# Kernel optimization log

Measured on AMD Instinct MI355X. Metric: run time of the kernel, lower is better.

## Reference

```python
import jax, jax.numpy as jnp
import numpy as np

B = 1024       # number of graphs in batch
N_T = 51200    # junction-tree nodes
N_G = 61440    # molecule atoms
E = 100352     # tree edges = line-graph nodes
E_LG = 200704  # line-graph edges
D = 450        # hidden / feature dim
VOCAB = 780    # junction-tree vocab


def _att(h, a, x, gid, nseg):
    # Attention.forward: per-graph softmax over node scores, weighted sum of x.
    q = (h @ a)[gid]                      # (N, d_x) query broadcast to nodes
    s = jnp.sum(x * q, axis=1)            # (N,)
    m = jax.ops.segment_max(s, gid, num_segments=nseg)
    e = jnp.exp(s - m[gid])
    z = jax.ops.segment_sum(e, gid, num_segments=nseg)
    return jax.ops.segment_sum((e / z[gid])[:, None] * x, gid, num_segments=nseg)


def setup_inputs() -> dict:
    key = jax.random.key(0)
    ks = iter(jax.random.split(key, 48))
    nk = lambda: next(ks)
    p = lambda shape: 0.001 * jax.random.uniform(nk(), shape, dtype=jnp.float32)
    inp = {}
    inp['x_T'] = jax.random.normal(nk(), (N_T, D), jnp.float32)
    inp['x_G'] = jax.random.normal(nk(), (N_G, D), jnp.float32)
    inp['id_onehot'] = jax.random.uniform(nk(), (N_T, VOCAB), dtype=jnp.float32)
    inp['msg0'] = jnp.zeros((E, D), jnp.float32)
    inp['embeddings'] = p((VOCAB, D))
    # TreeGRU params
    for n in ['wz', 'uz', 'wr', 'ur', 'w_h', 'u_h']:
        inp[n] = p((D, D))
    for n in ['bz', 'br', 'b_h']:
        inp[n] = jnp.zeros((1, D), jnp.float32)
    # decoder topology params
    inp['w_d1'] = p((D, D)); inp['w_d2'] = p((D, D)); inp['b_d1'] = jnp.zeros((1, D), jnp.float32)
    inp['a_dT'] = p((D, D)); inp['a_dG'] = p((D, D))
    inp['w_d3'] = p((D, D)); inp['w_d4'] = p((2 * D, D)); inp['b_d2'] = jnp.zeros((1, D), jnp.float32)
    inp['u_d'] = p((D, 1)); inp['b_d3'] = jnp.zeros((1,), jnp.float32)
    # decoder label params
    inp['w_l1'] = p((D, D)); inp['w_l2'] = p((2 * D, D)); inp['b_l1'] = jnp.zeros((1, D), jnp.float32)
    inp['a_lT'] = p((D, D)); inp['a_lG'] = p((D, D))
    inp['u_l'] = p((D, VOCAB)); inp['b_l2'] = jnp.zeros((1, VOCAB), jnp.float32)
    # targets
    inp['topo_target'] = (jax.random.uniform(nk(), (B,)) < 0.5).astype(jnp.float32)
    # graph structure (int)
    inp['edge_src'] = jax.random.randint(nk(), (E,), 0, N_T, jnp.int32)
    inp['edge_dst'] = jax.random.randint(nk(), (E,), 0, N_T, jnp.int32)
    inp['lg_src'] = jax.random.randint(nk(), (E_LG,), 0, E, jnp.int32)
    inp['lg_dst'] = jax.random.randint(nk(), (E_LG,), 0, E, jnp.int32)
    inp['gid_T'] = jnp.sort(jax.random.randint(nk(), (N_T,), 0, B, jnp.int32))
    inp['gid_G'] = jnp.sort(jax.random.randint(nk(), (N_G,), 0, B, jnp.int32))
    inp['root_eids'] = jax.random.randint(nk(), (B,), 0, E, jnp.int32)
    inp['label_target'] = jax.random.randint(nk(), (B,), 0, VOCAB, jnp.int32)
    return inp


def reference(x_T, x_G, id_onehot, msg0, embeddings, wz, uz, bz, wr, ur, br,
              w_h, u_h, b_h, w_d1, w_d2, b_d1, a_dT, a_dG, w_d3, w_d4, b_d2,
              u_d, b_d3, w_l1, w_l2, b_l1, a_lT, a_lG, u_l, b_l2, topo_target,
              edge_src, edge_dst, lg_src, lg_dst, gid_T, gid_G, root_eids,
              label_target):
    seg = jax.ops.segment_sum
    nE = msg0.shape[0]
    f = id_onehot @ embeddings            # Y_T.ndata['f']
    f_src = f[edge_src]                   # per line-graph-node source-node feat
    f_dst = f[edge_dst]
    # ---- TreeGRU over the line graph (full-graph update) ----
    s = seg(msg0[lg_src], lg_dst, num_segments=nE)                 # sum of h_{ki}
    z = jax.nn.sigmoid(f_src @ wz + s @ uz + bz)
    r = jax.nn.sigmoid(f_dst[lg_src] @ wr + msg0[lg_src] @ ur + br)  # per lg-edge
    sum_rh = seg(r * msg0[lg_src], lg_dst, num_segments=nE)
    h_tilde = jnp.tanh(f_src @ w_h + sum_rh @ u_h + b_h)
    msg = (1.0 - z) * s + z * h_tilde                               # new h_{ij}
    # ---- decoder hidden state per edge ----
    sum_h = seg(msg[lg_src], lg_dst, num_segments=nE)
    h = jax.nn.relu(f_src @ w_d1 + sum_h @ w_d2 + b_d1)             # (E, d_h)
    h_root = h[root_eids]                                           # (B, d_h)
    # ---- topology prediction (Eq. 5-6) ----
    c_d = jnp.concatenate([_att(h_root, a_dT, x_T, gid_T, B),
                           _att(h_root, a_dG, x_G, gid_G, B)], axis=1)
    d_logit = (jax.nn.relu(h_root @ w_d3 + c_d @ w_d4 + b_d2) @ u_d + b_d3)[:, 0]
    topology_ce = jnp.sum(jax.nn.softplus(d_logit) - topo_target * d_logit)
    # ---- label prediction (Eq. 8-9) ----
    q = msg[root_eids]                                              # (B, d_msgT)
    c_l = jnp.concatenate([_att(q, a_lT, x_T, gid_T, B),
                           _att(q, a_lG, x_G, gid_G, B)], axis=1)
    l_logits = jax.nn.relu(q @ w_l1 + c_l @ w_l2 + b_l1) @ u_l + b_l2
    lp = jax.nn.log_softmax(l_logits, axis=-1)
    label_ce = -jnp.sum(lp[jnp.arange(B), label_target])
    return jnp.stack([topology_ce, label_ce])
```

## Files before the change

### kernel.cpp

```cpp
#include <hip/hip_runtime.h>
#include <math.h>


#define BGR   1024
#define NT    51200
#define NG    61440
#define NE    100352
#define NELG  200704
#define D     450
#define DP    452
#define CATS  1356
#define VOCAB 780
#define VP    784
#define CAP   4096
#define KC    16
#define SAS   68
#define SWS   68

__device__ __forceinline__ float sigmoidf_(float x) { return 1.0f / (1.0f + expf(-x)); }
__device__ __forceinline__ float softplusf_(float x) {
    return fmaxf(x, 0.0f) + log1pf(expf(-fabsf(x)));
}
__device__ __forceinline__ int lower_bound_i(const int* __restrict__ a, int n, int v) {
    int lo = 0, hi = n;
    while (lo < hi) { int mid = (lo + hi) >> 1; if (a[mid] < v) lo = mid + 1; else hi = mid; }
    return lo;
}
__device__ __forceinline__ float4 g4(const float* p, bool pred) {
    float4 z = make_float4(0.f, 0.f, 0.f, 0.f);
    return pred ? *(const float4*)p : z;
}
__device__ __forceinline__ void loadb4a(const float* __restrict__ b, int c0, int n, float* o) {
#pragma unroll
    for (int i = 0; i < 4; ++i) o[i] = (c0 + i < n) ? b[c0 + i] : 0.f;
}

template <int M>
__device__ __forceinline__ void gemm64(
    const float* __restrict__ A, int ldA, int K, int rowBase, int nRows,
    const int* s_idx, const float* const (&W)[M], int ldW, int Wcols,
    int colBase, float* sA, float* sW, float (&acc)[M][4][4]) {
    const int tid = threadIdx.x;
    const int a_r = tid >> 2, a_k = (tid & 3) << 2;
    const int w_k = tid >> 4, w_c = (tid & 15) << 2;
    const int r0 = (tid & 15) << 2, c0 = (tid >> 4) << 2;
    const bool rok = (rowBase + a_r) < nRows;
    const float* arow;
    {
        int sr = rok ? (s_idx ? s_idx[a_r] : rowBase + a_r) : 0;
        arow = A + (size_t)sr * ldA;
    }
    const int wcol = colBase + w_c;
    const bool cok = (wcol < Wcols);
    const int nch = (K + KC - 1) / KC;
    float4 pa = g4(arow + a_k, rok && (a_k < K));
    float4 pw[M];
#pragma unroll
    for (int m = 0; m < M; ++m)
        pw[m] = g4(W[m] + (size_t)w_k * ldW + wcol, cok && (w_k < K));
    for (int ch = 0; ch < nch; ++ch) {
        __syncthreads();
        sA[(a_k + 0) * SAS + a_r] = pa.x;
        sA[(a_k + 1) * SAS + a_r] = pa.y;
        sA[(a_k + 2) * SAS + a_r] = pa.z;
        sA[(a_k + 3) * SAS + a_r] = pa.w;
#pragma unroll
        for (int m = 0; m < M; ++m)
            *(float4*)&sW[(m * KC + w_k) * SWS + w_c] = pw[m];
        __syncthreads();
        int k0 = (ch + 1) * KC;
        if (ch + 1 < nch) {
            pa = g4(arow + k0 + a_k, rok && (k0 + a_k < K));
#pragma unroll
            for (int m = 0; m < M; ++m)
                pw[m] = g4(W[m] + (size_t)(k0 + w_k) * ldW + wcol, cok && (k0 + w_k < K));
        }
#pragma unroll
        for (int k = 0; k < KC; ++k) {
            float4 av4 = *(const float4*)&sA[k * SAS + r0];
            float ar[4] = { av4.x, av4.y, av4.z, av4.w };
#pragma unroll
            for (int m = 0; m < M; ++m) {
                float4 wv4 = *(const float4*)&sW[(m * KC + k) * SWS + c0];
                float wr[4] = { wv4.x, wv4.y, wv4.z, wv4.w };
#pragma unroll
                for (int i = 0; i < 4; ++i)
#pragma unroll
                    for (int j = 0; j < 4; ++j)
                        acc[m][i][j] = fmaf(ar[i], wr[j], acc[m][i][j]);
            }
        }
    }
}

struct PrepJob { const float* src; float* dst; int srcRows; int srcCols; int ld; int cum; };
struct PrepArgs { PrepJob j[16]; int total; };

__global__ void k_prep(PrepArgs a) {
    int idx = blockIdx.x * blockDim.x + threadIdx.x;
    int stride = gridDim.x * blockDim.x;
    for (; idx < a.total; idx += stride) {
        int jj = 0;
        while (jj < 15 && idx >= a.j[jj + 1].cum) ++jj;
        PrepJob J = a.j[jj];
        int local = idx - J.cum;
        int row = local / J.ld, col = local - row * J.ld;
        float v = (row < J.srcRows && col < J.srcCols) ? J.src[(size_t)row * J.srcCols + col] : 0.f;
        J.dst[local] = v;
    }
}

__global__ void k_init(float* __restrict__ sumh, int* __restrict__ root_slot,
                       int* __restrict__ counter, float* __restrict__ dl,
                       float* __restrict__ out) {
    int i = blockIdx.x * blockDim.x + threadIdx.x;
    if (i < BGR * DP) sumh[i] = 0.0f;
    if (i < NE) root_slot[i] = -1;
    if (i < BGR) dl[i] = 0.0f;
    if (i == 0) counter[0] = 0;
    if (i < 2) out[i] = 0.0f;
}

__global__ void k_scatter_roots(const int* __restrict__ root_eids, int* __restrict__ root_slot) {
    int b = blockIdx.x * blockDim.x + threadIdx.x;
    if (b < BGR) root_slot[root_eids[b]] = b;
}

__global__ void k_build_tasks(const int* __restrict__ lg_src, const int* __restrict__ lg_dst,
                              const int* __restrict__ edge_src, const int* __restrict__ root_slot,
                              int2* __restrict__ tasks, int* __restrict__ counter) {
    int j = blockIdx.x * blockDim.x + threadIdx.x;
    if (j < NELG) {
        int r = root_slot[lg_dst[j]];
        if (r >= 0) {
            int idx = atomicAdd(counter, 1);
            if (idx < CAP) tasks[idx] = make_int2(edge_src[lg_src[j]], r);
        }
    }
}

__global__ __launch_bounds__(256) void kA(
    const float* __restrict__ id_onehot, const float* __restrict__ emb_p,
    const int* __restrict__ edge_src, const int* __restrict__ root_eids,
    const int2* __restrict__ tasks, const int* __restrict__ counter,
    float* __restrict__ f_all) {
    __shared__ float sA[KC * SAS];
    __shared__ float sW[KC * SWS];
    __shared__ int s_idx[64];
    int T = counter[0]; if (T > CAP) T = CAP;
    int nRows = BGR + T;
    int rowBase = blockIdx.x * 64, colBase = blockIdx.y * 64;
    if (rowBase >= nRows) return;
    int tid = threadIdx.x;
    if (tid < 64) {
        int row = rowBase + tid, n = 0;
        if (row < nRows) n = (row < BGR) ? edge_src[root_eids[row]] : tasks[row - BGR].x;
        s_idx[tid] = n;
    }
    __syncthreads();
    float acc[1][4][4] = {};
    const float* W[1] = { emb_p };
    gemm64<1>(id_onehot, VOCAB, VOCAB, rowBase, nRows, s_idx, W, DP, DP, colBase, sA, sW, acc);
    int r0 = (tid & 15) << 2, c0 = (tid >> 4) << 2;
    int cg = colBase + c0;
    if (cg < DP) {
#pragma unroll
        for (int i = 0; i < 4; ++i) {
            int row = rowBase + r0 + i;
            if (row < nRows)
                *(float4*)(f_all + (size_t)row * DP + cg) =
                    make_float4(acc[0][i][0], acc[0][i][1], acc[0][i][2], acc[0][i][3]);
        }
    }
}

__global__ __launch_bounds__(256) void kB(
    const float* __restrict__ f_all,
    const float* __restrict__ wz_p, const float* __restrict__ wh_p, const float* __restrict__ wd1_p,
    const float* __restrict__ bz, const float* __restrict__ b_h,
    const int2* __restrict__ tasks, const int* __restrict__ counter,
    float* __restrict__ catl, float* __restrict__ fw1, float* __restrict__ sumh) {
    __shared__ float sA[KC * SAS];
    __shared__ float sW[3 * KC * SWS];
    int tileR = blockIdx.x, colBase = blockIdx.y * 64;
    int tid = threadIdx.x;
    int r0 = (tid & 15) << 2, c0 = (tid >> 4) << 2;
    int cg = colBase + c0;
    int T = counter[0]; if (T > CAP) T = CAP;
    if (tileR < 16) {
        int rowBase = tileR * 64;
        float acc[3][4][4] = {};
        const float* W[3] = { wz_p, wh_p, wd1_p };
        gemm64<3>(f_all, DP, DP, rowBase, BGR, nullptr, W, DP, DP, colBase, sA, sW, acc);
        if (cg < DP) {
            float bz4[4], bh4[4];
            loadb4a(bz, cg, D, bz4); loadb4a(b_h, cg, D, bh4);
#pragma unroll
            for (int i = 0; i < 4; ++i) {
                int row = rowBase + r0 + i;
                float q[4];
#pragma unroll
                for (int j = 0; j < 4; ++j)
                    q[j] = sigmoidf_(acc[0][i][j] + bz4[j]) * tanhf(acc[1][i][j] + bh4[j]);
                *(float4*)(catl + (size_t)row * CATS + cg) = make_float4(q[0], q[1], q[2], q[3]);
                *(float4*)(fw1 + (size_t)row * DP + cg) =
                    make_float4(acc[2][i][0], acc[2][i][1], acc[2][i][2], acc[2][i][3]);
            }
        }
    } else {
        int rowBase = BGR + (tileR - 16) * 64;
        int nRows = BGR + T;
        if (rowBase >= nRows) return;
        float acc[2][4][4] = {};
        const float* W[2] = { wz_p, wh_p };
        gemm64<2>(f_all, DP, DP, rowBase, nRows, nullptr, W, DP, DP, colBase, sA, sW, acc);
        if (cg < DP) {
            float bz4[4], bh4[4];
            loadb4a(bz, cg, D, bz4); loadb4a(b_h, cg, D, bh4);
#pragma unroll
            for (int i = 0; i < 4; ++i) {
                int row = rowBase + r0 + i;
                if (row < nRows) {
                    int slot = tasks[row - BGR].y;
                    float* dst = sumh + (size_t)slot * DP + cg;
#pragma unroll
                    for (int j = 0; j < 4; ++j)
                        atomicAdd(dst + j, sigmoidf_(acc[0][i][j] + bz4[j]) * tanhf(acc[1][i][j] + bh4[j]));
                }
            }
        }
    }
}

__global__ __launch_bounds__(256) void kC(
    const float* __restrict__ fw1, const float* __restrict__ sumh,
    const int* __restrict__ root_slot, const int* __restrict__ root_eids,
    const float* __restrict__ wd2_p, const float* __restrict__ b_d1,
    float* __restrict__ catd) {
    __shared__ float sA[KC * SAS];
    __shared__ float sW[KC * SWS];
    __shared__ int s_idx[64];
    int rowBase = blockIdx.x * 64, colBase = blockIdx.y * 64;
    int tid = threadIdx.x;
    if (tid < 64) s_idx[tid] = root_slot[root_eids[rowBase + tid]];
    __syncthreads();
    float acc[1][4][4] = {};
    const float* W[1] = { wd2_p };
    gemm64<1>(sumh, DP, DP, rowBase, BGR, s_idx, W, DP, DP, colBase, sA, sW, acc);
    int r0 = (tid & 15) << 2, c0 = (tid >> 4) << 2;
    int cg = colBase + c0;
    if (cg < DP) {
        float bd[4]; loadb4a(b_d1, cg, D, bd);
#pragma unroll
        for (int i = 0; i < 4; ++i) {
            int row = rowBase + r0 + i;
            float4 f1 = *(const float4*)(fw1 + (size_t)row * DP + cg);
            float fr[4] = { f1.x, f1.y, f1.z, f1.w };
            float o[4];
#pragma unroll
            for (int j = 0; j < 4; ++j) o[j] = fmaxf(acc[0][i][j] + fr[j] + bd[j], 0.f);
            *(float4*)(catd + (size_t)row * CATS + cg) = make_float4(o[0], o[1], o[2], o[3]);
        }
    }
}

__global__ __launch_bounds__(256) void kD(
    const float* __restrict__ catd, const float* __restrict__ catl,
    const float* __restrict__ adT_p, const float* __restrict__ adG_p,
    const float* __restrict__ alT_p, const float* __restrict__ alG_p,
    float* __restrict__ qdT, float* __restrict__ qdG,
    float* __restrict__ qlT, float* __restrict__ qlG) {
    __shared__ float sA[KC * SAS];
    __shared__ float sW[2 * KC * SWS];
    int rowBase = blockIdx.x * 64, colBase = blockIdx.y * 64, job = blockIdx.z;
    int tid = threadIdx.x;
    const float* A = job ? catl : catd;
    float acc[2][4][4] = {};
    const float* W[2] = { job ? alT_p : adT_p, job ? alG_p : adG_p };
    gemm64<2>(A, CATS, DP, rowBase, BGR, nullptr, W, DP, DP, colBase, sA, sW, acc);
    int r0 = (tid & 15) << 2, c0 = (tid >> 4) << 2;
    int cg = colBase + c0;
    if (cg < DP) {
        float* oa = job ? qlT : qdT;
        float* ob = job ? qlG : qdG;
#pragma unroll
        for (int i = 0; i < 4; ++i) {
            int row = rowBase + r0 + i;
            *(float4*)(oa + (size_t)row * DP + cg) =
                make_float4(acc[0][i][0], acc[0][i][1], acc[0][i][2], acc[0][i][3]);
            *(float4*)(ob + (size_t)row * DP + cg) =
                make_float4(acc[1][i][0], acc[1][i][1], acc[1][i][2], acc[1][i][3]);
        }
    }
}

__global__ __launch_bounds__(256) void k_att(
    const float* __restrict__ x_T, const float* __restrict__ x_G,
    const int* __restrict__ gid_T, const int* __restrict__ gid_G,
    const float* __restrict__ qdT, const float* __restrict__ qdG,
    const float* __restrict__ qlT, const float* __restrict__ qlG,
    float* __restrict__ catd, float* __restrict__ catl) {
    int bid = blockIdx.x, b = bid & (BGR - 1), which = bid >> 10;
    const float* x   = which ? x_G   : x_T;
    const int*   gid = which ? gid_G : gid_T;
    int N            = which ? NG    : NT;
    const float* qd  = (which ? qdG : qdT) + (size_t)b * DP;
    const float* ql  = (which ? qlG : qlT) + (size_t)b * DP;
    float* ad = catd + (size_t)b * CATS + DP + which * DP;
    float* al = catl + (size_t)b * CATS + DP + which * DP;
    int tid = threadIdx.x, lane = tid & 63, wave = tid >> 6;
    __shared__ float s_qd[D], s_ql[D];
    __shared__ float s_m[4][2], s_z[4][2];
    __shared__ float s_acc[4][2][D];
    for (int d = tid; d < D; d += 256) { s_qd[d] = qd[d]; s_ql[d] = ql[d]; }
    int lo = lower_bound_i(gid, N, b), hi = lower_bound_i(gid, N, b + 1);
    __syncthreads();
    float md = -INFINITY, ml = -INFINITY, zd = 0.0f, zl = 0.0f;
    float accd[8] = {}, accl[8] = {};
    for (int n = lo + wave; n < hi; n += 4) {
        const float* xr = x + (size_t)n * D;
        float vx[8]; float pd = 0.0f, pl = 0.0f;
#pragma unroll
        for (int i = 0; i < 8; ++i) {
            int d = lane + (i << 6);
            float v = (d < D) ? xr[d] : 0.0f;
            vx[i] = v;
            if (d < D) { pd = fmaf(v, s_qd[d], pd); pl = fmaf(v, s_ql[d], pl); }
        }
#pragma unroll
        for (int o = 32; o; o >>= 1) { pd += __shfl_xor(pd, o); pl += __shfl_xor(pl, o); }
        float nmd = fmaxf(md, pd), nml = fmaxf(ml, pl);
        float sd = expf(md - nmd), sl = expf(ml - nml);
        float ed = expf(pd - nmd), el = expf(pl - nml);
        zd = zd * sd + ed; zl = zl * sl + el;
#pragma unroll
        for (int i = 0; i < 8; ++i) {
            accd[i] = fmaf(accd[i], sd, ed * vx[i]);
            accl[i] = fmaf(accl[i], sl, el * vx[i]);
        }
        md = nmd; ml = nml;
    }
#pragma unroll
    for (int i = 0; i < 8; ++i) {
        int d = lane + (i << 6);
        if (d < D) { s_acc[wave][0][d] = accd[i]; s_acc[wave][1][d] = accl[i]; }
    }
    if (lane == 0) { s_m[wave][0] = md; s_m[wave][1] = ml; s_z[wave][0] = zd; s_z[wave][1] = zl; }
    __syncthreads();
    bool nonempty = (hi > lo);
    float Md = fmaxf(fmaxf(s_m[0][0], s_m[1][0]), fmaxf(s_m[2][0], s_m[3][0]));
    float Ml = fmaxf(fmaxf(s_m[0][1], s_m[1][1]), fmaxf(s_m[2][1], s_m[3][1]));
    float scd[4], scl[4];
#pragma unroll
    for (int w = 0; w < 4; ++w) { scd[w] = expf(s_m[w][0] - Md); scl[w] = expf(s_m[w][1] - Ml); }
    float Zd = s_z[0][0] * scd[0] + s_z[1][0] * scd[1] + s_z[2][0] * scd[2] + s_z[3][0] * scd[3];
    float Zl = s_z[0][1] * scl[0] + s_z[1][1] * scl[1] + s_z[2][1] * scl[2] + s_z[3][1] * scl[3];
    for (int d = tid; d < DP; d += 256) {
        bool v = (d < D);
        float adv = 0.f, alv = 0.f;
        if (v && nonempty) {
            adv = (s_acc[0][0][d] * scd[0] + s_acc[1][0][d] * scd[1]
                 + s_acc[2][0][d] * scd[2] + s_acc[3][0][d] * scd[3]) / Zd;
            alv = (s_acc[0][1][d] * scl[0] + s_acc[1][1][d] * scl[1]
                 + s_acc[2][1][d] * scl[2] + s_acc[3][1][d] * scl[3]) / Zl;
        }
        ad[d] = adv; al[d] = alv;
    }
}

__global__ __launch_bounds__(256) void kEF(
    const float* __restrict__ catd, const float* __restrict__ catl,
    const float* __restrict__ wcd_p, const float* __restrict__ wcl_p,
    const float* __restrict__ b_d2, const float* __restrict__ u_d,
    const float* __restrict__ b_l1,
    float* __restrict__ h_l, float* __restrict__ dl) {
    __shared__ float sA[KC * SAS];
    __shared__ float sW[KC * SWS];
    __shared__ float s_dl[64];
    int rowBase = blockIdx.x * 64, colBase = blockIdx.y * 64, job = blockIdx.z;
    int tid = threadIdx.x;
    if (!job && tid < 64) s_dl[tid] = 0.f;
    float acc[1][4][4] = {};
    const float* A = job ? catl : catd;
    const float* W[1] = { job ? wcl_p : wcd_p };
    gemm64<1>(A, CATS, CATS, rowBase, BGR, nullptr, W, DP, DP, colBase, sA, sW, acc);
    int r0 = (tid & 15) << 2, c0 = (tid >> 4) << 2;
    int cg = colBase + c0;
    if (job) {
        if (cg < DP) {
            float b1[4]; loadb4a(b_l1, cg, D, b1);
#pragma unroll
            for (int i = 0; i < 4; ++i) {
                int row = rowBase + r0 + i;
                *(float4*)(h_l + (size_t)row * DP + cg) =
                    make_float4(fmaxf(acc[0][i][0] + b1[0], 0.f), fmaxf(acc[0][i][1] + b1[1], 0.f),
                                fmaxf(acc[0][i][2] + b1[2], 0.f), fmaxf(acc[0][i][3] + b1[3], 0.f));
            }
        }
    } else {
        if (cg < DP) {
            float b2[4], ud[4];
            loadb4a(b_d2, cg, D, b2); loadb4a(u_d, cg, D, ud);
#pragma unroll
            for (int i = 0; i < 4; ++i) {
                float p = 0.f;
#pragma unroll
                for (int j = 0; j < 4; ++j) p += fmaxf(acc[0][i][j] + b2[j], 0.f) * ud[j];
                atomicAdd(&s_dl[r0 + i], p);
            }
        }
        __syncthreads();
        if (tid < 64) atomicAdd(&dl[rowBase + tid], s_dl[tid]);
    }
}

__global__ __launch_bounds__(256) void kG(
    const float* __restrict__ h_l, const float* __restrict__ ul_p,
    const float* __restrict__ b_l2, float* __restrict__ logits) {
    __shared__ float sA[KC * SAS];
    __shared__ float sW[KC * SWS];
    int rowBase = blockIdx.x * 64, colBase = blockIdx.y * 64;
    int tid = threadIdx.x;
    float acc[1][4][4] = {};
    const float* W[1] = { ul_p };
    gemm64<1>(h_l, DP, DP, rowBase, BGR, nullptr, W, VP, VP, colBase, sA, sW, acc);
    int r0 = (tid & 15) << 2, c0 = (tid >> 4) << 2;
    int cg = colBase + c0;
    if (cg < VP) {
        float bl[4]; loadb4a(b_l2, cg, VOCAB, bl);
#pragma unroll
        for (int i = 0; i < 4; ++i) {
            int row = rowBase + r0 + i;
            *(float4*)(logits + (size_t)row * VP + cg) =
                make_float4(acc[0][i][0] + bl[0], acc[0][i][1] + bl[1],
                            acc[0][i][2] + bl[2], acc[0][i][3] + bl[3]);
        }
    }
}

__global__ __launch_bounds__(256) void k_ce(
    const float* __restrict__ logits, const int* __restrict__ label_t,
    float* __restrict__ out) {
    __shared__ float s_red[4];
    int base = blockIdx.x * 4, tid = threadIdx.x, lane = tid & 63, wave = tid >> 6;
    float ce = 0.0f;
    for (int r = 0; r < 4; ++r) {
        const float* lg = logits + (size_t)(base + r) * VP;
        float m = -INFINITY;
        for (int d = tid; d < VOCAB; d += 256) m = fmaxf(m, lg[d]);
#pragma unroll
        for (int o = 32; o; o >>= 1) m = fmaxf(m, __shfl_xor(m, o));
        if (lane == 0) s_red[wave] = m;
        __syncthreads();
        float m4 = fmaxf(fmaxf(s_red[0], s_red[1]), fmaxf(s_red[2], s_red[3]));
        __syncthreads();
        float s = 0.0f;
        for (int d = tid; d < VOCAB; d += 256) s += expf(lg[d] - m4);
#pragma unroll
        for (int o = 32; o; o >>= 1) s += __shfl_xor(s, o);
        if (lane == 0) s_red[wave] = s;
        __syncthreads();
        if (tid == 0) {
            float Z = s_red[0] + s_red[1] + s_red[2] + s_red[3];
            ce += (m4 + logf(Z)) - lg[label_t[base + r]];
        }
        __syncthreads();
    }
    if (tid == 0) atomicAdd(&out[1], ce);
}

__global__ __launch_bounds__(1024) void k_topo_final(
    const float* __restrict__ dl, const float* __restrict__ b_d3,
    const float* __restrict__ topo_t, float* __restrict__ out) {
    __shared__ float s_red[16];
    int tid = threadIdx.x, lane = tid & 63, wave = tid >> 6;
    float v = dl[tid] + b_d3[0];
    float ce = softplusf_(v) - topo_t[tid] * v;
#pragma unroll
    for (int o = 32; o; o >>= 1) ce += __shfl_xor(ce, o);
    if (lane == 0) s_red[wave] = ce;
    __syncthreads();
    if (tid == 0) {
        float s = 0.f;
#pragma unroll
        for (int w = 0; w < 16; ++w) s += s_red[w];
        atomicAdd(&out[0], s);
    }
}

extern "C" void kernel_launch(void* const* d_in, const int* in_sizes, int n_in,
                              void* d_out, int out_size, void* d_ws, size_t ws_size,
                              hipStream_t stream) {
    const float* x_T       = (const float*)d_in[0];
    const float* x_G       = (const float*)d_in[1];
    const float* id_onehot = (const float*)d_in[2];
    const float* emb   = (const float*)d_in[4];
    const float* wz    = (const float*)d_in[5];
    const float* w_h   = (const float*)d_in[9];
    const float* bz    = (const float*)d_in[11];
    const float* b_h   = (const float*)d_in[13];
    const float* w_d1  = (const float*)d_in[14];
    const float* w_d2  = (const float*)d_in[15];
    const float* b_d1  = (const float*)d_in[16];
    const float* a_dT  = (const float*)d_in[17];
    const float* a_dG  = (const float*)d_in[18];
    const float* w_d3  = (const float*)d_in[19];
    const float* w_d4  = (const float*)d_in[20];
    const float* b_d2  = (const float*)d_in[21];
    const float* u_d   = (const float*)d_in[22];
    const float* b_d3  = (const float*)d_in[23];
    const float* w_l1  = (const float*)d_in[24];
    const float* w_l2  = (const float*)d_in[25];
    const float* b_l1  = (const float*)d_in[26];
    const float* a_lT  = (const float*)d_in[27];
    const float* a_lG  = (const float*)d_in[28];
    const float* u_l   = (const float*)d_in[29];
    const float* b_l2  = (const float*)d_in[30];
    const float* topo_t = (const float*)d_in[31];
    const int* edge_src  = (const int*)d_in[32];
    const int* lg_src    = (const int*)d_in[34];
    const int* lg_dst    = (const int*)d_in[35];
    const int* gid_T     = (const int*)d_in[36];
    const int* gid_G     = (const int*)d_in[37];
    const int* root_eids = (const int*)d_in[38];
    const int* label_t   = (const int*)d_in[39];
    float* out = (float*)d_out;

    char* p = (char*)d_ws;
    auto take = [&](size_t bytes) -> char* {
        char* r = p; p += (bytes + 255) & ~(size_t)255; return r;
    };
    const size_t WSQ = (size_t)DP * DP * 4;
    float* wz_p  = (float*)take(WSQ);
    float* wh_p  = (float*)take(WSQ);
    float* wd1_p = (float*)take(WSQ);
    float* wd2_p = (float*)take(WSQ);
    float* adT_p = (float*)take(WSQ);
    float* adG_p = (float*)take(WSQ);
    float* alT_p = (float*)take(WSQ);
    float* alG_p = (float*)take(WSQ);
    float* wcd_p = (float*)take((size_t)CATS * DP * 4);
    float* wcl_p = (float*)take((size_t)CATS * DP * 4);
    float* emb_p = (float*)take((size_t)VOCAB * DP * 4);
    float* ul_p  = (float*)take((size_t)DP * VP * 4);
    float* catd  = (float*)take((size_t)BGR * CATS * 4);
    float* catl  = (float*)take((size_t)BGR * CATS * 4);
    float* f_all = (float*)take((size_t)(BGR + CAP) * DP * 4);
    const size_t BD = (size_t)BGR * DP * 4;
    float* fw1  = (float*)take(BD);
    float* sumh = (float*)take(BD);
    float* h_l  = (float*)take(BD);
    float* qdT  = (float*)take(BD);
    float* qdG  = (float*)take(BD);
    float* qlT  = (float*)take(BD);
    float* qlG  = (float*)take(BD);
    float* logits = qdT;
    float* dl   = (float*)take((size_t)BGR * 4);
    int*  root_slot = (int*)take((size_t)NE * 4);
    int*  counter   = (int*)take(256);
    int2* tasks     = (int2*)take((size_t)CAP * 8);

    PrepArgs pa; int cum = 0;
    auto addjob = [&](int i, const float* src, float* dst, int sr, int sc, int dr, int ld) {
        pa.j[i].src = src; pa.j[i].dst = dst; pa.j[i].srcRows = sr; pa.j[i].srcCols = sc;
        pa.j[i].ld = ld; pa.j[i].cum = cum; cum += dr * ld;
    };
    addjob(0, wz, wz_p, D, D, DP, DP);
    addjob(1, w_h, wh_p, D, D, DP, DP);
    addjob(2, w_d1, wd1_p, D, D, DP, DP);
    addjob(3, w_d2, wd2_p, D, D, DP, DP);
    addjob(4, a_dT, adT_p, D, D, DP, DP);
    addjob(5, a_dG, adG_p, D, D, DP, DP);
    addjob(6, a_lT, alT_p, D, D, DP, DP);
    addjob(7, a_lG, alG_p, D, D, DP, DP);
    addjob(8, w_d3, wcd_p, D, D, DP, DP);
    addjob(9, w_d4, wcd_p + (size_t)DP * DP, D, D, DP, DP);
    addjob(10, w_d4 + (size_t)D * D, wcd_p + (size_t)2 * DP * DP, D, D, DP, DP);
    addjob(11, w_l1, wcl_p, D, D, DP, DP);
    addjob(12, w_l2, wcl_p + (size_t)DP * DP, D, D, DP, DP);
    addjob(13, w_l2 + (size_t)D * D, wcl_p + (size_t)2 * DP * DP, D, D, DP, DP);
    addjob(14, emb, emb_p, VOCAB, D, VOCAB, DP);
    addjob(15, u_l, ul_p, D, VOCAB, DP, VP);
    pa.total = cum;

    k_prep<<<2048, 256, 0, stream>>>(pa);
    k_init<<<(BGR * DP + 255) / 256, 256, 0, stream>>>(sumh, root_slot, counter, dl, out);
    k_scatter_roots<<<(BGR + 255) / 256, 256, 0, stream>>>(root_eids, root_slot);
    k_build_tasks<<<(NELG + 255) / 256, 256, 0, stream>>>(lg_src, lg_dst, edge_src, root_slot, tasks, counter);
    kA<<<dim3((BGR + CAP) / 64, 8), 256, 0, stream>>>(id_onehot, emb_p, edge_src, root_eids,
                                                      tasks, counter, f_all);
    kB<<<dim3(16 + CAP / 64, 8), 256, 0, stream>>>(f_all, wz_p, wh_p, wd1_p, bz, b_h,
                                                   tasks, counter, catl, fw1, sumh);
    kC<<<dim3(16, 8), 256, 0, stream>>>(fw1, sumh, root_slot, root_eids, wd2_p, b_d1, catd);
    kD<<<dim3(16, 8, 2), 256, 0, stream>>>(catd, catl, adT_p, adG_p, alT_p, alG_p,
                                           qdT, qdG, qlT, qlG);
    k_att<<<2 * BGR, 256, 0, stream>>>(x_T, x_G, gid_T, gid_G, qdT, qdG, qlT, qlG, catd, catl);
    kEF<<<dim3(16, 8, 2), 256, 0, stream>>>(catd, catl, wcd_p, wcl_p, b_d2, u_d, b_l1, h_l, dl);
    k_topo_final<<<1, 1024, 0, stream>>>(dl, b_d3, topo_t, out);
    kG<<<dim3(16, VP / 64 + 1, 1), 256, 0, stream>>>(h_l, ul_p, b_l2, logits);
    k_ce<<<BGR / 4, 256, 0, stream>>>(logits, label_t, out);
}
```

Baseline: 941.6 us.

## Replace FP32 SIMT GEMMs with split-bf16 MFMA matrix-core GEMMs

Every dense GEMM stage moves from the shared-memory FP32 FMA tiling to MFMA 16x16x32 bf16 instructions. To keep near-FP32 accuracy, each operand is split into hi and lo bf16 parts and three products are accumulated. Weights are pre-transposed and padded into bf16 hi/lo buffers, and activations are converted the same way between stages. This adds extra conversion kernels and memory traffic, and the MFMA loop reads operands directly from global memory with no LDS staging.

```diff
diff --git a/kernel.cpp b/kernel.cpp
--- a/kernel.cpp
+++ b/kernel.cpp
@@ -9,13 +9,17 @@
 #define NELG  200704
 #define D     450
 #define DP    452
-#define CATS  1356
+#define KP_D  480
+#define KP_V  800
+#define CATP  1440
 #define VOCAB 780
 #define VP    784
 #define CAP   4096
-#define KC    16
-#define SAS   68
-#define SWS   68
+#define WT_N  512
+#define WT_NV 832
+
+typedef short bf16x8 __attribute__((ext_vector_type(8)));
+typedef float f32x4 __attribute__((ext_vector_type(4)));
 
 __device__ __forceinline__ float sigmoidf_(float x) { return 1.0f / (1.0f + expf(-x)); }
 __device__ __forceinline__ float softplusf_(float x) {
@@ -26,87 +30,68 @@
     while (lo < hi) { int mid = (lo + hi) >> 1; if (a[mid] < v) lo = mid + 1; else hi = mid; }
     return lo;
 }
-__device__ __forceinline__ float4 g4(const float* p, bool pred) {
-    float4 z = make_float4(0.f, 0.f, 0.f, 0.f);
-    return pred ? *(const float4*)p : z;
-}
-__device__ __forceinline__ void loadb4a(const float* __restrict__ b, int c0, int n, float* o) {
-#pragma unroll
-    for (int i = 0; i < 4; ++i) o[i] = (c0 + i < n) ? b[c0 + i] : 0.f;
-}
-
-template <int M>
-__device__ __forceinline__ void gemm64(
-    const float* __restrict__ A, int ldA, int K, int rowBase, int nRows,
-    const int* s_idx, const float* const (&W)[M], int ldW, int Wcols,
-    int colBase, float* sA, float* sW, float (&acc)[M][4][4]) {
-    const int tid = threadIdx.x;
-    const int a_r = tid >> 2, a_k = (tid & 3) << 2;
-    const int w_k = tid >> 4, w_c = (tid & 15) << 2;
-    const int r0 = (tid & 15) << 2, c0 = (tid >> 4) << 2;
-    const bool rok = (rowBase + a_r) < nRows;
-    const float* arow;
-    {
-        int sr = rok ? (s_idx ? s_idx[a_r] : rowBase + a_r) : 0;
-        arow = A + (size_t)sr * ldA;
-    }
-    const int wcol = colBase + w_c;
-    const bool cok = (wcol < Wcols);
-    const int nch = (K + KC - 1) / KC;
-    float4 pa = g4(arow + a_k, rok && (a_k < K));
-    float4 pw[M];
-#pragma unroll
-    for (int m = 0; m < M; ++m)
-        pw[m] = g4(W[m] + (size_t)w_k * ldW + wcol, cok && (w_k < K));
-    for (int ch = 0; ch < nch; ++ch) {
-        __syncthreads();
-        sA[(a_k + 0) * SAS + a_r] = pa.x;
-        sA[(a_k + 1) * SAS + a_r] = pa.y;
-        sA[(a_k + 2) * SAS + a_r] = pa.z;
-        sA[(a_k + 3) * SAS + a_r] = pa.w;
-#pragma unroll
-        for (int m = 0; m < M; ++m)
-            *(float4*)&sW[(m * KC + w_k) * SWS + w_c] = pw[m];
-        __syncthreads();
-        int k0 = (ch + 1) * KC;
-        if (ch + 1 < nch) {
-            pa = g4(arow + k0 + a_k, rok && (k0 + a_k < K));
-#pragma unroll
-            for (int m = 0; m < M; ++m)
-                pw[m] = g4(W[m] + (size_t)(k0 + w_k) * ldW + wcol, cok && (k0 + w_k < K));
-        }
-#pragma unroll
-        for (int k = 0; k < KC; ++k) {
-            float4 av4 = *(const float4*)&sA[k * SAS + r0];
-            float ar[4] = { av4.x, av4.y, av4.z, av4.w };
-#pragma unroll
-            for (int m = 0; m < M; ++m) {
-                float4 wv4 = *(const float4*)&sW[(m * KC + k) * SWS + c0];
-                float wr[4] = { wv4.x, wv4.y, wv4.z, wv4.w };
-#pragma unroll
-                for (int i = 0; i < 4; ++i)
-#pragma unroll
-                    for (int j = 0; j < 4; ++j)
-                        acc[m][i][j] = fmaf(ar[i], wr[j], acc[m][i][j]);
-            }
-        }
-    }
-}
-
-struct PrepJob { const float* src; float* dst; int srcRows; int srcCols; int ld; int cum; };
-struct PrepArgs { PrepJob j[16]; int total; };
-
-__global__ void k_prep(PrepArgs a) {
+__device__ __forceinline__ unsigned short f2bf(float x) {
+    unsigned u = __float_as_uint(x);
+    unsigned r = (u + 0x7FFFu + ((u >> 16) & 1u)) >> 16;
+    return (unsigned short)r;
+}
+__device__ __forceinline__ float bf2f(unsigned short h) {
+    return __uint_as_float(((unsigned)h) << 16);
+}
+__device__ __forceinline__ void split2(float x, unsigned short& h, unsigned short& l) {
+    h = f2bf(x); l = f2bf(x - bf2f(h));
+}
+__device__ __forceinline__ float dot4(float4 a, float4 b) {
+    return fmaf(a.x, b.x, fmaf(a.y, b.y, fmaf(a.z, b.z, a.w * b.w)));
+}
+
+__device__ __forceinline__ void mfma_strip(
+    const unsigned short* __restrict__ Ah, const unsigned short* __restrict__ Al,
+    int ldA, int rowStrip,
+    const unsigned short* __restrict__ Wh, const unsigned short* __restrict__ Wl,
+    int ldW, int colBase, int Kp, f32x4 (&acc)[4]) {
+    int lane = threadIdx.x & 63, m = lane & 15, q = lane >> 4;
+    const unsigned short* pah = Ah + (size_t)(rowStrip + m) * ldA + q * 8;
+    const unsigned short* pal = Al + (size_t)(rowStrip + m) * ldA + q * 8;
+    const unsigned short* pwh[4]; const unsigned short* pwl[4];
+#pragma unroll
+    for (int c = 0; c < 4; ++c) {
+        int col = colBase + c * 16 + m;
+        pwh[c] = Wh + (size_t)col * ldW + q * 8;
+        pwl[c] = Wl + (size_t)col * ldW + q * 8;
+    }
+#pragma unroll 2
+    for (int k0 = 0; k0 < Kp; k0 += 32) {
+        bf16x8 aH = *(const bf16x8*)(pah + k0);
+        bf16x8 aL = *(const bf16x8*)(pal + k0);
+#pragma unroll
+        for (int c = 0; c < 4; ++c) {
+            bf16x8 bH = *(const bf16x8*)(pwh[c] + k0);
+            bf16x8 bL = *(const bf16x8*)(pwl[c] + k0);
+            acc[c] = __builtin_amdgcn_mfma_f32_16x16x32_bf16(aH, bH, acc[c], 0, 0, 0);
+            acc[c] = __builtin_amdgcn_mfma_f32_16x16x32_bf16(aH, bL, acc[c], 0, 0, 0);
+            acc[c] = __builtin_amdgcn_mfma_f32_16x16x32_bf16(aL, bH, acc[c], 0, 0, 0);
+        }
+    }
+}
+
+struct WJob { const float* src; int srcK, srcN, Kp, kOff, kLen, NA, dstOff, cum; };
+struct WArgs { WJob j[16]; int total; };
+
+__global__ void k_prepw(WArgs a, unsigned short* __restrict__ whi,
+                        unsigned short* __restrict__ wlo) {
     int idx = blockIdx.x * blockDim.x + threadIdx.x;
     int stride = gridDim.x * blockDim.x;
     for (; idx < a.total; idx += stride) {
         int jj = 0;
         while (jj < 15 && idx >= a.j[jj + 1].cum) ++jj;
-        PrepJob J = a.j[jj];
+        WJob J = a.j[jj];
         int local = idx - J.cum;
-        int row = local / J.ld, col = local - row * J.ld;
-        float v = (row < J.srcRows && col < J.srcCols) ? J.src[(size_t)row * J.srcCols + col] : 0.f;
-        J.dst[local] = v;
+        int col = local / J.kLen, kk = local - col * J.kLen;
+        float v = (kk < J.srcK && col < J.srcN) ? J.src[(size_t)kk * J.srcN + col] : 0.f;
+        unsigned short h, l; split2(v, h, l);
+        size_t pos = (size_t)J.dstOff + (size_t)col * J.Kp + J.kOff + kk;
+        whi[pos] = h; wlo[pos] = l;
     }
 }
 
@@ -139,157 +124,192 @@
     }
 }
 
-__global__ __launch_bounds__(256) void kA(
-    const float* __restrict__ id_onehot, const float* __restrict__ emb_p,
-    const int* __restrict__ edge_src, const int* __restrict__ root_eids,
-    const int2* __restrict__ tasks, const int* __restrict__ counter,
-    float* __restrict__ f_all) {
-    __shared__ float sA[KC * SAS];
-    __shared__ float sW[KC * SWS];
-    __shared__ int s_idx[64];
+__global__ void k_gather_idoh(
+    const float* __restrict__ id_onehot, const int* __restrict__ edge_src,
+    const int* __restrict__ root_eids, const int2* __restrict__ tasks,
+    const int* __restrict__ counter,
+    unsigned short* __restrict__ ih, unsigned short* __restrict__ il) {
     int T = counter[0]; if (T > CAP) T = CAP;
     int nRows = BGR + T;
-    int rowBase = blockIdx.x * 64, colBase = blockIdx.y * 64;
-    if (rowBase >= nRows) return;
-    int tid = threadIdx.x;
-    if (tid < 64) {
-        int row = rowBase + tid, n = 0;
-        if (row < nRows) n = (row < BGR) ? edge_src[root_eids[row]] : tasks[row - BGR].x;
-        s_idx[tid] = n;
-    }
-    __syncthreads();
-    float acc[1][4][4] = {};
-    const float* W[1] = { emb_p };
-    gemm64<1>(id_onehot, VOCAB, VOCAB, rowBase, nRows, s_idx, W, DP, DP, colBase, sA, sW, acc);
-    int r0 = (tid & 15) << 2, c0 = (tid >> 4) << 2;
-    int cg = colBase + c0;
-    if (cg < DP) {
-#pragma unroll
-        for (int i = 0; i < 4; ++i) {
-            int row = rowBase + r0 + i;
-            if (row < nRows)
-                *(float4*)(f_all + (size_t)row * DP + cg) =
-                    make_float4(acc[0][i][0], acc[0][i][1], acc[0][i][2], acc[0][i][3]);
+    long total = (long)(BGR + CAP) * KP_V;
+    long idx = (long)(blockIdx.x * blockDim.x + threadIdx.x);
+    long stride = (long)gridDim.x * blockDim.x;
+    for (; idx < total; idx += stride) {
+        int row = (int)(idx / KP_V), k = (int)(idx - (long)row * KP_V);
+        float v = 0.f;
+        if (row < nRows && k < VOCAB) {
+            int n = (row < BGR) ? edge_src[root_eids[row]] : tasks[row - BGR].x;
+            v = id_onehot[(size_t)n * VOCAB + k];
+        }
+        unsigned short h, l; split2(v, h, l);
+        ih[idx] = h; il[idx] = l;
+    }
+}
+
+__global__ void k_conv_sumh(
+    const float* __restrict__ sumh, const int* __restrict__ root_slot,
+    const int* __restrict__ root_eids,
+    unsigned short* __restrict__ sh, unsigned short* __restrict__ sl) {
+    int idx = blockIdx.x * blockDim.x + threadIdx.x;
+    if (idx >= BGR * KP_D) return;
+    int b = idx / KP_D, k = idx - b * KP_D;
+    int slot = root_slot[root_eids[b]];
+    float v = (k < D) ? sumh[(size_t)slot * DP + k] : 0.f;
+    unsigned short h, l; split2(v, h, l);
+    sh[idx] = h; sl[idx] = l;
+}
+
+__global__ __launch_bounds__(256) void kA(
+    const unsigned short* __restrict__ ih, const unsigned short* __restrict__ il,
+    const unsigned short* __restrict__ eTh, const unsigned short* __restrict__ eTl,
+    const int* __restrict__ counter,
+    unsigned short* __restrict__ fH, unsigned short* __restrict__ fL) {
+    int T = counter[0]; if (T > CAP) T = CAP;
+    int nRows = BGR + T;
+    int rowBase = blockIdx.x * 64; if (rowBase >= nRows) return;
+    int colBase = blockIdx.y * 64;
+    int rowStrip = rowBase + (threadIdx.x >> 6) * 16;
+    f32x4 z4 = {0.f, 0.f, 0.f, 0.f};
+    f32x4 acc[4] = {z4, z4, z4, z4};
+    mfma_strip(ih, il, KP_V, rowStrip, eTh, eTl, KP_V, colBase, KP_V, acc);
+    int lane = threadIdx.x & 63, mI = lane & 15, q = lane >> 4;
+#pragma unroll
+    for (int c = 0; c < 4; ++c) {
+        int col = colBase + c * 16 + mI;
+        if (col >= KP_D) continue;
+#pragma unroll
+        for (int r = 0; r < 4; ++r) {
+            int row = rowStrip + q * 4 + r;
+            unsigned short h, l; split2(acc[c][r], h, l);
+            fH[(size_t)row * KP_D + col] = h;
+            fL[(size_t)row * KP_D + col] = l;
         }
     }
 }
 
 __global__ __launch_bounds__(256) void kB(
-    const float* __restrict__ f_all,
-    const float* __restrict__ wz_p, const float* __restrict__ wh_p, const float* __restrict__ wd1_p,
+    const unsigned short* __restrict__ fH, const unsigned short* __restrict__ fL,
+    const unsigned short* __restrict__ wzTh, const unsigned short* __restrict__ wzTl,
+    const unsigned short* __restrict__ whTh, const unsigned short* __restrict__ whTl,
     const float* __restrict__ bz, const float* __restrict__ b_h,
     const int2* __restrict__ tasks, const int* __restrict__ counter,
-    float* __restrict__ catl, float* __restrict__ fw1, float* __restrict__ sumh) {
-    __shared__ float sA[KC * SAS];
-    __shared__ float sW[3 * KC * SWS];
-    int tileR = blockIdx.x, colBase = blockIdx.y * 64;
-    int tid = threadIdx.x;
-    int r0 = (tid & 15) << 2, c0 = (tid >> 4) << 2;
-    int cg = colBase + c0;
+    unsigned short* __restrict__ clH, unsigned short* __restrict__ clL,
+    float* __restrict__ sumh) {
     int T = counter[0]; if (T > CAP) T = CAP;
-    if (tileR < 16) {
-        int rowBase = tileR * 64;
-        float acc[3][4][4] = {};
-        const float* W[3] = { wz_p, wh_p, wd1_p };
-        gemm64<3>(f_all, DP, DP, rowBase, BGR, nullptr, W, DP, DP, colBase, sA, sW, acc);
-        if (cg < DP) {
-            float bz4[4], bh4[4];
-            loadb4a(bz, cg, D, bz4); loadb4a(b_h, cg, D, bh4);
-#pragma unroll
-            for (int i = 0; i < 4; ++i) {
-                int row = rowBase + r0 + i;
-                float q[4];
-#pragma unroll
-                for (int j = 0; j < 4; ++j)
-                    q[j] = sigmoidf_(acc[0][i][j] + bz4[j]) * tanhf(acc[1][i][j] + bh4[j]);
-                *(float4*)(catl + (size_t)row * CATS + cg) = make_float4(q[0], q[1], q[2], q[3]);
-                *(float4*)(fw1 + (size_t)row * DP + cg) =
-                    make_float4(acc[2][i][0], acc[2][i][1], acc[2][i][2], acc[2][i][3]);
+    int nRows = BGR + T;
+    int rowBase = blockIdx.x * 64; if (rowBase >= nRows) return;
+    int colBase = blockIdx.y * 64;
+    int rowStrip = rowBase + (threadIdx.x >> 6) * 16;
+    f32x4 z4 = {0.f, 0.f, 0.f, 0.f};
+    f32x4 accZ[4] = {z4, z4, z4, z4};
+    f32x4 accH[4] = {z4, z4, z4, z4};
+    mfma_strip(fH, fL, KP_D, rowStrip, wzTh, wzTl, KP_D, colBase, KP_D, accZ);
+    mfma_strip(fH, fL, KP_D, rowStrip, whTh, whTl, KP_D, colBase, KP_D, accH);
+    int lane = threadIdx.x & 63, mI = lane & 15, q = lane >> 4;
+    bool isRoot = rowBase < BGR;
+#pragma unroll
+    for (int c = 0; c < 4; ++c) {
+        int col = colBase + c * 16 + mI;
+        if (col >= KP_D) continue;
+        float bzv = (col < D) ? bz[col] : 0.f;
+        float bhv = (col < D) ? b_h[col] : 0.f;
+#pragma unroll
+        for (int r = 0; r < 4; ++r) {
+            int row = rowStrip + q * 4 + r;
+            float v = (col < D) ? sigmoidf_(accZ[c][r] + bzv) * tanhf(accH[c][r] + bhv) : 0.f;
+            if (isRoot) {
+                unsigned short h, l; split2(v, h, l);
+                clH[(size_t)row * CATP + col] = h;
+                clL[(size_t)row * CATP + col] = l;
+            } else if (row < nRows && col < D) {
+                int slot = tasks[row - BGR].y;
+                atomicAdd(&sumh[(size_t)slot * DP + col], v);
             }
         }
-    } else {
-        int rowBase = BGR + (tileR - 16) * 64;
-        int nRows = BGR + T;
-        if (rowBase >= nRows) return;
-        float acc[2][4][4] = {};
-        const float* W[2] = { wz_p, wh_p };
-        gemm64<2>(f_all, DP, DP, rowBase, nRows, nullptr, W, DP, DP, colBase, sA, sW, acc);
-        if (cg < DP) {
-            float bz4[4], bh4[4];
-            loadb4a(bz, cg, D, bz4); loadb4a(b_h, cg, D, bh4);
-#pragma unroll
-            for (int i = 0; i < 4; ++i) {
-                int row = rowBase + r0 + i;
-                if (row < nRows) {
-                    int slot = tasks[row - BGR].y;
-                    float* dst = sumh + (size_t)slot * DP + cg;
-#pragma unroll
-                    for (int j = 0; j < 4; ++j)
-                        atomicAdd(dst + j, sigmoidf_(acc[0][i][j] + bz4[j]) * tanhf(acc[1][i][j] + bh4[j]));
-                }
-            }
-        }
+    }
+}
+
+__global__ __launch_bounds__(256) void kB2(
+    const unsigned short* __restrict__ fH, const unsigned short* __restrict__ fL,
+    const unsigned short* __restrict__ wTh, const unsigned short* __restrict__ wTl,
+    float* __restrict__ fw1) {
+    int rowStrip = blockIdx.x * 64 + (threadIdx.x >> 6) * 16;
+    int colBase = blockIdx.y * 64;
+    f32x4 z4 = {0.f, 0.f, 0.f, 0.f};
+    f32x4 acc[4] = {z4, z4, z4, z4};
+    mfma_strip(fH, fL, KP_D, rowStrip, wTh, wTl, KP_D, colBase, KP_D, acc);
+    int lane = threadIdx.x & 63, mI = lane & 15, q = lane >> 4;
+#pragma unroll
+    for (int c = 0; c < 4; ++c) {
+        int col = colBase + c * 16 + mI;
+        if (col >= D) continue;
+#pragma unroll
+        for (int r = 0; r < 4; ++r)
+            fw1[(size_t)(rowStrip + q * 4 + r) * DP + col] = acc[c][r];
     }
 }
 
 __global__ __launch_bounds__(256) void kC(
-    const float* __restrict__ fw1, const float* __restrict__ sumh,
-    const int* __restrict__ root_slot, const int* __restrict__ root_eids,
-    const float* __restrict__ wd2_p, const float* __restrict__ b_d1,
-    float* __restrict__ catd) {
-    __shared__ float sA[KC * SAS];
-    __shared__ float sW[KC * SWS];
-    __shared__ int s_idx[64];
-    int rowBase = blockIdx.x * 64, colBase = blockIdx.y * 64;
-    int tid = threadIdx.x;
-    if (tid < 64) s_idx[tid] = root_slot[root_eids[rowBase + tid]];
-    __syncthreads();
-    float acc[1][4][4] = {};
-    const float* W[1] = { wd2_p };
-    gemm64<1>(sumh, DP, DP, rowBase, BGR, s_idx, W, DP, DP, colBase, sA, sW, acc);
-    int r0 = (tid & 15) << 2, c0 = (tid >> 4) << 2;
-    int cg = colBase + c0;
-    if (cg < DP) {
-        float bd[4]; loadb4a(b_d1, cg, D, bd);
-#pragma unroll
-        for (int i = 0; i < 4; ++i) {
-            int row = rowBase + r0 + i;
-            float4 f1 = *(const float4*)(fw1 + (size_t)row * DP + cg);
-            float fr[4] = { f1.x, f1.y, f1.z, f1.w };
-            float o[4];
-#pragma unroll
-            for (int j = 0; j < 4; ++j) o[j] = fmaxf(acc[0][i][j] + fr[j] + bd[j], 0.f);
-            *(float4*)(catd + (size_t)row * CATS + cg) = make_float4(o[0], o[1], o[2], o[3]);
+    const unsigned short* __restrict__ sH, const unsigned short* __restrict__ sL,
+    const unsigned short* __restrict__ wTh, const unsigned short* __restrict__ wTl,
+    const float* __restrict__ fw1, const float* __restrict__ b_d1,
+    unsigned short* __restrict__ cdH, unsigned short* __restrict__ cdL) {
+    int rowStrip = blockIdx.x * 64 + (threadIdx.x >> 6) * 16;
+    int colBase = blockIdx.y * 64;
+    f32x4 z4 = {0.f, 0.f, 0.f, 0.f};
+    f32x4 acc[4] = {z4, z4, z4, z4};
+    mfma_strip(sH, sL, KP_D, rowStrip, wTh, wTl, KP_D, colBase, KP_D, acc);
+    int lane = threadIdx.x & 63, mI = lane & 15, q = lane >> 4;
+#pragma unroll
+    for (int c = 0; c < 4; ++c) {
+        int col = colBase + c * 16 + mI;
+        if (col >= KP_D) continue;
+        float bd = (col < D) ? b_d1[col] : 0.f;
+#pragma unroll
+        for (int r = 0; r < 4; ++r) {
+            int row = rowStrip + q * 4 + r;
+            float v = 0.f;
+            if (col < D)
+                v = fmaxf(fw1[(size_t)row * DP + col] + acc[c][r] + bd, 0.f);
+            unsigned short h, l; split2(v, h, l);
+            cdH[(size_t)row * CATP + col] = h;
+            cdL[(size_t)row * CATP + col] = l;
         }
     }
 }
 
 __global__ __launch_bounds__(256) void kD(
-    const float* __restrict__ catd, const float* __restrict__ catl,
-    const float* __restrict__ adT_p, const float* __restrict__ adG_p,
-    const float* __restrict__ alT_p, const float* __restrict__ alG_p,
+    const unsigned short* __restrict__ cdH, const unsigned short* __restrict__ cdL,
+    const unsigned short* __restrict__ clH, const unsigned short* __restrict__ clL,
+    const unsigned short* __restrict__ aTh0, const unsigned short* __restrict__ aTl0,
+    const unsigned short* __restrict__ aGh0, const unsigned short* __restrict__ aGl0,
+    const unsigned short* __restrict__ aTh1, const unsigned short* __restrict__ aTl1,
+    const unsigned short* __restrict__ aGh1, const unsigned short* __restrict__ aGl1,
     float* __restrict__ qdT, float* __restrict__ qdG,
     float* __restrict__ qlT, float* __restrict__ qlG) {
-    __shared__ float sA[KC * SAS];
-    __shared__ float sW[2 * KC * SWS];
-    int rowBase = blockIdx.x * 64, colBase = blockIdx.y * 64, job = blockIdx.z;
-    int tid = threadIdx.x;
-    const float* A = job ? catl : catd;
-    float acc[2][4][4] = {};
-    const float* W[2] = { job ? alT_p : adT_p, job ? alG_p : adG_p };
-    gemm64<2>(A, CATS, DP, rowBase, BGR, nullptr, W, DP, DP, colBase, sA, sW, acc);
-    int r0 = (tid & 15) << 2, c0 = (tid >> 4) << 2;
-    int cg = colBase + c0;
-    if (cg < DP) {
-        float* oa = job ? qlT : qdT;
-        float* ob = job ? qlG : qdG;
-#pragma unroll
-        for (int i = 0; i < 4; ++i) {
-            int row = rowBase + r0 + i;
-            *(float4*)(oa + (size_t)row * DP + cg) =
-                make_float4(acc[0][i][0], acc[0][i][1], acc[0][i][2], acc[0][i][3]);
-            *(float4*)(ob + (size_t)row * DP + cg) =
-                make_float4(acc[1][i][0], acc[1][i][1], acc[1][i][2], acc[1][i][3]);
+    int rowStrip = blockIdx.x * 64 + (threadIdx.x >> 6) * 16;
+    int colBase = blockIdx.y * 64, job = blockIdx.z;
+    const unsigned short* Ah = job ? clH : cdH;
+    const unsigned short* Al = job ? clL : cdL;
+    f32x4 z4 = {0.f, 0.f, 0.f, 0.f};
+    f32x4 accT[4] = {z4, z4, z4, z4};
+    f32x4 accG[4] = {z4, z4, z4, z4};
+    mfma_strip(Ah, Al, CATP, rowStrip, job ? aTh1 : aTh0, job ? aTl1 : aTl0,
+               KP_D, colBase, KP_D, accT);
+    mfma_strip(Ah, Al, CATP, rowStrip, job ? aGh1 : aGh0, job ? aGl1 : aGl0,
+               KP_D, colBase, KP_D, accG);
+    float* oT = job ? qlT : qdT;
+    float* oG = job ? qlG : qdG;
+    int lane = threadIdx.x & 63, mI = lane & 15, q = lane >> 4;
+#pragma unroll
+    for (int c = 0; c < 4; ++c) {
+        int col = colBase + c * 16 + mI;
+        if (col >= D) continue;
+#pragma unroll
+        for (int r = 0; r < 4; ++r) {
+            int row = rowStrip + q * 4 + r;
+            oT[(size_t)row * DP + col] = accT[c][r];
+            oG[(size_t)row * DP + col] = accG[c][r];
         }
     }
 }
@@ -299,52 +319,68 @@
     const int* __restrict__ gid_T, const int* __restrict__ gid_G,
     const float* __restrict__ qdT, const float* __restrict__ qdG,
     const float* __restrict__ qlT, const float* __restrict__ qlG,
-    float* __restrict__ catd, float* __restrict__ catl) {
+    unsigned short* __restrict__ cdH, unsigned short* __restrict__ cdL,
+    unsigned short* __restrict__ clH, unsigned short* __restrict__ clL) {
     int bid = blockIdx.x, b = bid & (BGR - 1), which = bid >> 10;
     const float* x   = which ? x_G   : x_T;
     const int*   gid = which ? gid_G : gid_T;
     int N            = which ? NG    : NT;
     const float* qd  = (which ? qdG : qdT) + (size_t)b * DP;
     const float* ql  = (which ? qlG : qlT) + (size_t)b * DP;
-    float* ad = catd + (size_t)b * CATS + DP + which * DP;
-    float* al = catl + (size_t)b * CATS + DP + which * DP;
+    size_t segOff = (size_t)b * CATP + 480 + which * 480;
     int tid = threadIdx.x, lane = tid & 63, wave = tid >> 6;
-    __shared__ float s_qd[D], s_ql[D];
+    __shared__ __align__(16) float s_qd[DP], s_ql[DP];
     __shared__ float s_m[4][2], s_z[4][2];
-    __shared__ float s_acc[4][2][D];
-    for (int d = tid; d < D; d += 256) { s_qd[d] = qd[d]; s_ql[d] = ql[d]; }
+    __shared__ __align__(16) float s_acc[4][2][DP];
+    for (int d = tid; d < DP; d += 256) {
+        s_qd[d] = (d < D) ? qd[d] : 0.f;
+        s_ql[d] = (d < D) ? ql[d] : 0.f;
+    }
     int lo = lower_bound_i(gid, N, b), hi = lower_bound_i(gid, N, b + 1);
     __syncthreads();
-    float md = -INFINITY, ml = -INFINITY, zd = 0.0f, zl = 0.0f;
-    float accd[8] = {}, accl[8] = {};
+    int g0 = lane, g1 = 64 + lane;
+    bool g1ok = g1 < 112;
+    bool tok = (lane == 48) || (lane == 49);
+    int td = 448 + (lane - 48);
+    float4 qd0 = *(const float4*)&s_qd[4 * g0];
+    float4 ql0 = *(const float4*)&s_ql[4 * g0];
+    float4 qd1 = g1ok ? *(const float4*)&s_qd[4 * g1] : make_float4(0, 0, 0, 0);
+    float4 ql1 = g1ok ? *(const float4*)&s_ql[4 * g1] : make_float4(0, 0, 0, 0);
+    float tqd = tok ? s_qd[td] : 0.f, tql = tok ? s_ql[td] : 0.f;
+    float md = -INFINITY, ml = -INFINITY, zd = 0.f, zl = 0.f;
+    float4 ad0 = make_float4(0, 0, 0, 0), ad1 = ad0, al0 = ad0, al1 = ad0;
+    float atd = 0.f, atl = 0.f;
     for (int n = lo + wave; n < hi; n += 4) {
         const float* xr = x + (size_t)n * D;
-        float vx[8]; float pd = 0.0f, pl = 0.0f;
-#pragma unroll
-        for (int i = 0; i < 8; ++i) {
-            int d = lane + (i << 6);
-            float v = (d < D) ? xr[d] : 0.0f;
-            vx[i] = v;
-            if (d < D) { pd = fmaf(v, s_qd[d], pd); pl = fmaf(v, s_ql[d], pl); }
-        }
+        float4 v0 = *(const float4*)(xr + 4 * g0);
+        float4 v1 = g1ok ? *(const float4*)(xr + 4 * g1) : make_float4(0, 0, 0, 0);
+        float tv = tok ? xr[td] : 0.f;
+        float pd = dot4(v0, qd0) + dot4(v1, qd1) + tv * tqd;
+        float pl = dot4(v0, ql0) + dot4(v1, ql1) + tv * tql;
 #pragma unroll
         for (int o = 32; o; o >>= 1) { pd += __shfl_xor(pd, o); pl += __shfl_xor(pl, o); }
         float nmd = fmaxf(md, pd), nml = fmaxf(ml, pl);
         float sd = expf(md - nmd), sl = expf(ml - nml);
         float ed = expf(pd - nmd), el = expf(pl - nml);
         zd = zd * sd + ed; zl = zl * sl + el;
-#pragma unroll
-        for (int i = 0; i < 8; ++i) {
-            accd[i] = fmaf(accd[i], sd, ed * vx[i]);
-            accl[i] = fmaf(accl[i], sl, el * vx[i]);
-        }
+        ad0.x = ad0.x * sd + ed * v0.x; ad0.y = ad0.y * sd + ed * v0.y;
+        ad0.z = ad0.z * sd + ed * v0.z; ad0.w = ad0.w * sd + ed * v0.w;
+        ad1.x = ad1.x * sd + ed * v1.x; ad1.y = ad1.y * sd + ed * v1.y;
+        ad1.z = ad1.z * sd + ed * v1.z; ad1.w = ad1.w * sd + ed * v1.w;
+        al0.x = al0.x * sl + el * v0.x; al0.y = al0.y * sl + el * v0.y;
+        al0.z = al0.z * sl + el * v0.z; al0.w = al0.w * sl + el * v0.w;
+        al1.x = al1.x * sl + el * v1.x; al1.y = al1.y * sl + el * v1.y;
+        al1.z = al1.z * sl + el * v1.z; al1.w = al1.w * sl + el * v1.w;
+        atd = atd * sd + ed * tv; atl = atl * sl + el * tv;
         md = nmd; ml = nml;
     }
-#pragma unroll
-    for (int i = 0; i < 8; ++i) {
-        int d = lane + (i << 6);
-        if (d < D) { s_acc[wave][0][d] = accd[i]; s_acc[wave][1][d] = accl[i]; }
-    }
+    *(float4*)&s_acc[wave][0][4 * g0] = ad0;
+    *(float4*)&s_acc[wave][1][4 * g0] = al0;
+    if (g1ok) {
+        *(float4*)&s_acc[wave][0][4 * g1] = ad1;
+        *(float4*)&s_acc[wave][1][4 * g1] = al1;
+    }
+    if (tok) { s_acc[wave][0][td] = atd; s_acc[wave][1][td] = atl; }
     if (lane == 0) { s_m[wave][0] = md; s_m[wave][1] = ml; s_z[wave][0] = zd; s_z[wave][1] = zl; }
     __syncthreads();
     bool nonempty = (hi > lo);
@@ -355,86 +391,86 @@
     for (int w = 0; w < 4; ++w) { scd[w] = expf(s_m[w][0] - Md); scl[w] = expf(s_m[w][1] - Ml); }
     float Zd = s_z[0][0] * scd[0] + s_z[1][0] * scd[1] + s_z[2][0] * scd[2] + s_z[3][0] * scd[3];
     float Zl = s_z[0][1] * scl[0] + s_z[1][1] * scl[1] + s_z[2][1] * scl[2] + s_z[3][1] * scl[3];
-    for (int d = tid; d < DP; d += 256) {
-        bool v = (d < D);
-        float adv = 0.f, alv = 0.f;
-        if (v && nonempty) {
-            adv = (s_acc[0][0][d] * scd[0] + s_acc[1][0][d] * scd[1]
-                 + s_acc[2][0][d] * scd[2] + s_acc[3][0][d] * scd[3]) / Zd;
-            alv = (s_acc[0][1][d] * scl[0] + s_acc[1][1][d] * scl[1]
-                 + s_acc[2][1][d] * scl[2] + s_acc[3][1][d] * scl[3]) / Zl;
-        }
-        ad[d] = adv; al[d] = alv;
+    for (int d = tid; d < KP_D; d += 256) {
+        float av = 0.f, lv = 0.f;
+        if (d < D && nonempty) {
+            av = (s_acc[0][0][d] * scd[0] + s_acc[1][0][d] * scd[1]
+                + s_acc[2][0][d] * scd[2] + s_acc[3][0][d] * scd[3]) / Zd;
+            lv = (s_acc[0][1][d] * scl[0] + s_acc[1][1][d] * scl[1]
+                + s_acc[2][1][d] * scl[2] + s_acc[3][1][d] * scl[3]) / Zl;
+        }
+        unsigned short h, l;
+        split2(av, h, l); cdH[segOff + d] = h; cdL[segOff + d] = l;
+        split2(lv, h, l); clH[segOff + d] = h; clL[segOff + d] = l;
     }
 }
 
 __global__ __launch_bounds__(256) void kEF(
-    const float* __restrict__ catd, const float* __restrict__ catl,
-    const float* __restrict__ wcd_p, const float* __restrict__ wcl_p,
+    const unsigned short* __restrict__ cdH, const unsigned short* __restrict__ cdL,
+    const unsigned short* __restrict__ clH, const unsigned short* __restrict__ clL,
+    const unsigned short* __restrict__ wdTh, const unsigned short* __restrict__ wdTl,
+    const unsigned short* __restrict__ wlTh, const unsigned short* __restrict__ wlTl,
     const float* __restrict__ b_d2, const float* __restrict__ u_d,
     const float* __restrict__ b_l1,
-    float* __restrict__ h_l, float* __restrict__ dl) {
-    __shared__ float sA[KC * SAS];
-    __shared__ float sW[KC * SWS];
-    __shared__ float s_dl[64];
-    int rowBase = blockIdx.x * 64, colBase = blockIdx.y * 64, job = blockIdx.z;
-    int tid = threadIdx.x;
-    if (!job && tid < 64) s_dl[tid] = 0.f;
-    float acc[1][4][4] = {};
-    const float* A = job ? catl : catd;
-    const float* W[1] = { job ? wcl_p : wcd_p };
-    gemm64<1>(A, CATS, CATS, rowBase, BGR, nullptr, W, DP, DP, colBase, sA, sW, acc);
-    int r0 = (tid & 15) << 2, c0 = (tid >> 4) << 2;
-    int cg = colBase + c0;
+    unsigned short* __restrict__ hlH, unsigned short* __restrict__ hlL,
+    float* __restrict__ dl) {
+    int rowStrip = blockIdx.x * 64 + (threadIdx.x >> 6) * 16;
+    int colBase = blockIdx.y * 64, job = blockIdx.z;
+    f32x4 z4 = {0.f, 0.f, 0.f, 0.f};
+    f32x4 acc[4] = {z4, z4, z4, z4};
+    mfma_strip(job ? clH : cdH, job ? clL : cdL, CATP, rowStrip,
+               job ? wlTh : wdTh, job ? wlTl : wdTl, CATP, colBase, CATP, acc);
+    int lane = threadIdx.x & 63, mI = lane & 15, q = lane >> 4;
     if (job) {
-        if (cg < DP) {
-            float b1[4]; loadb4a(b_l1, cg, D, b1);
-#pragma unroll
-            for (int i = 0; i < 4; ++i) {
-                int row = rowBase + r0 + i;
-                *(float4*)(h_l + (size_t)row * DP + cg) =
-                    make_float4(fmaxf(acc[0][i][0] + b1[0], 0.f), fmaxf(acc[0][i][1] + b1[1], 0.f),
-                                fmaxf(acc[0][i][2] + b1[2], 0.f), fmaxf(acc[0][i][3] + b1[3], 0.f));
+#pragma unroll
+        for (int c = 0; c < 4; ++c) {
+            int col = colBase + c * 16 + mI;
+            if (col >= KP_D) continue;
+            float b1 = (col < D) ? b_l1[col] : 0.f;
+#pragma unroll
+            for (int r = 0; r < 4; ++r) {
+                int row = rowStrip + q * 4 + r;
+                float v = (col < D) ? fmaxf(acc[c][r] + b1, 0.f) : 0.f;
+                unsigned short h, l; split2(v, h, l);
+                hlH[(size_t)row * KP_D + col] = h;
+                hlL[(size_t)row * KP_D + col] = l;
             }
         }
     } else {
-        if (cg < DP) {
-            float b2[4], ud[4];
-            loadb4a(b_d2, cg, D, b2); loadb4a(u_d, cg, D, ud);
-#pragma unroll
-            for (int i = 0; i < 4; ++i) {
-                float p = 0.f;
-#pragma unroll
-                for (int j = 0; j < 4; ++j) p += fmaxf(acc[0][i][j] + b2[j], 0.f) * ud[j];
-                atomicAdd(&s_dl[r0 + i], p);
+#pragma unroll
+        for (int r = 0; r < 4; ++r) {
+            float pr = 0.f;
+#pragma unroll
+            for (int c = 0; c < 4; ++c) {
+                int col = colBase + c * 16 + mI;
+                if (col < D)
+                    pr += fmaxf(acc[c][r] + b_d2[col], 0.f) * u_d[col];
             }
-        }
-        __syncthreads();
-        if (tid < 64) atomicAdd(&dl[rowBase + tid], s_dl[tid]);
+#pragma unroll
+            for (int o = 1; o < 16; o <<= 1) pr += __shfl_xor(pr, o);
+            if (mI == 0) atomicAdd(&dl[rowStrip + q * 4 + r], pr);
+        }
     }
 }
 
 __global__ __launch_bounds__(256) void kG(
-    const float* __restrict__ h_l, const float* __restrict__ ul_p,
+    const unsigned short* __restrict__ hlH, const unsigned short* __restrict__ hlL,
+    const unsigned short* __restrict__ uTh, const unsigned short* __restrict__ uTl,
     const float* __restrict__ b_l2, float* __restrict__ logits) {
-    __shared__ float sA[KC * SAS];
-    __shared__ float sW[KC * SWS];
-    int rowBase = blockIdx.x * 64, colBase = blockIdx.y * 64;
-    int tid = threadIdx.x;
-    float acc[1][4][4] = {};
-    const float* W[1] = { ul_p };
-    gemm64<1>(h_l, DP, DP, rowBase, BGR, nullptr, W, VP, VP, colBase, sA, sW, acc);
-    int r0 = (tid & 15) << 2, c0 = (tid >> 4) << 2;
-    int cg = colBase + c0;
-    if (cg < VP) {
-        float bl[4]; loadb4a(b_l2, cg, VOCAB, bl);
-#pragma unroll
-        for (int i = 0; i < 4; ++i) {
-            int row = rowBase + r0 + i;
-            *(float4*)(logits + (size_t)row * VP + cg) =
-                make_float4(acc[0][i][0] + bl[0], acc[0][i][1] + bl[1],
-                            acc[0][i][2] + bl[2], acc[0][i][3] + bl[3]);
-        }
+    int rowStrip = blockIdx.x * 64 + (threadIdx.x >> 6) * 16;
+    int colBase = blockIdx.y * 64;
+    f32x4 z4 = {0.f, 0.f, 0.f, 0.f};
+    f32x4 acc[4] = {z4, z4, z4, z4};
+    mfma_strip(hlH, hlL, KP_D, rowStrip, uTh, uTl, KP_D, colBase, KP_D, acc);
+    int lane = threadIdx.x & 63, mI = lane & 15, q = lane >> 4;
+#pragma unroll
+    for (int c = 0; c < 4; ++c) {
+        int col = colBase + c * 16 + mI;
+        if (col >= VOCAB) continue;
+        float bl = b_l2[col];
+#pragma unroll
+        for (int r = 0; r < 4; ++r)
+            logits[(size_t)(rowStrip + q * 4 + r) * VP + col] = acc[c][r] + bl;
     }
 }
 
@@ -530,73 +566,91 @@
     auto take = [&](size_t bytes) -> char* {
         char* r = p; p += (bytes + 255) & ~(size_t)255; return r;
     };
-    const size_t WSQ = (size_t)DP * DP * 4;
-    float* wz_p  = (float*)take(WSQ);
-    float* wh_p  = (float*)take(WSQ);
-    float* wd1_p = (float*)take(WSQ);
-    float* wd2_p = (float*)take(WSQ);
-    float* adT_p = (float*)take(WSQ);
-    float* adG_p = (float*)take(WSQ);
-    float* alT_p = (float*)take(WSQ);
-    float* alG_p = (float*)take(WSQ);
-    float* wcd_p = (float*)take((size_t)CATS * DP * 4);
-    float* wcl_p = (float*)take((size_t)CATS * DP * 4);
-    float* emb_p = (float*)take((size_t)VOCAB * DP * 4);
-    float* ul_p  = (float*)take((size_t)DP * VP * 4);
-    float* catd  = (float*)take((size_t)BGR * CATS * 4);
-    float* catl  = (float*)take((size_t)BGR * CATS * 4);
-    float* f_all = (float*)take((size_t)(BGR + CAP) * DP * 4);
+    typedef unsigned short u16;
+    const int SQ = WT_N * KP_D;
+    const int oWZ = 0, oWH = oWZ + SQ, oWD1 = oWH + SQ, oWD2 = oWD1 + SQ;
+    const int oADT = oWD2 + SQ, oADG = oADT + SQ, oALT = oADG + SQ, oALG = oALT + SQ;
+    const int oWCD = oALG + SQ;
+    const int oWCL = oWCD + WT_N * CATP;
+    const int oEMB = oWCL + WT_N * CATP;
+    const int oUL  = oEMB + WT_N * KP_V;
+    const int oEND = oUL + WT_NV * KP_D;
+    u16* whi = (u16*)take((size_t)oEND * 2);
+    u16* wlo = (u16*)take((size_t)oEND * 2);
+    u16* idohH = (u16*)take((size_t)(BGR + CAP) * KP_V * 2);
+    u16* idohL = (u16*)take((size_t)(BGR + CAP) * KP_V * 2);
+    u16* fH    = (u16*)take((size_t)(BGR + CAP) * KP_D * 2);
+    u16* fL    = (u16*)take((size_t)(BGR + CAP) * KP_D * 2);
+    u16* sH    = (u16*)take((size_t)BGR * KP_D * 2);
+    u16* sL    = (u16*)take((size_t)BGR * KP_D * 2);
+    u16* cdH   = (u16*)take((size_t)BGR * CATP * 2);
+    u16* cdL   = (u16*)take((size_t)BGR * CATP * 2);
+    u16* clH   = (u16*)take((size_t)BGR * CATP * 2);
+    u16* clL   = (u16*)take((size_t)BGR * CATP * 2);
+    u16* hlH   = (u16*)take((size_t)BGR * KP_D * 2);
+    u16* hlL   = (u16*)take((size_t)BGR * KP_D * 2);
     const size_t BD = (size_t)BGR * DP * 4;
-    float* fw1  = (float*)take(BD);
-    float* sumh = (float*)take(BD);
-    float* h_l  = (float*)take(BD);
-    float* qdT  = (float*)take(BD);
-    float* qdG  = (float*)take(BD);
-    float* qlT  = (float*)take(BD);
-    float* qlG  = (float*)take(BD);
-    float* logits = qdT;
-    float* dl   = (float*)take((size_t)BGR * 4);
+    float* sumh  = (float*)take(BD);
+    float* fw1   = (float*)take(BD);
+    float* qdT   = (float*)take(BD);
+    float* qdG   = (float*)take(BD);
+    float* qlT   = (float*)take(BD);
+    float* qlG   = (float*)take(BD);
+    float* logits = (float*)take((size_t)BGR * VP * 4);
+    float* dl    = (float*)take((size_t)BGR * 4);
     int*  root_slot = (int*)take((size_t)NE * 4);
     int*  counter   = (int*)take(256);
     int2* tasks     = (int2*)take((size_t)CAP * 8);
 
-    PrepArgs pa; int cum = 0;
-    auto addjob = [&](int i, const float* src, float* dst, int sr, int sc, int dr, int ld) {
-        pa.j[i].src = src; pa.j[i].dst = dst; pa.j[i].srcRows = sr; pa.j[i].srcCols = sc;
-        pa.j[i].ld = ld; pa.j[i].cum = cum; cum += dr * ld;
+    WArgs wa; int cum = 0;
+    auto addw = [&](int i, const float* src, int srcK, int srcN, int Kp, int kOff,
+                    int kLen, int NA, int dstOff) {
+        wa.j[i] = WJob{src, srcK, srcN, Kp, kOff, kLen, NA, dstOff, cum};
+        cum += NA * kLen;
     };
-    addjob(0, wz, wz_p, D, D, DP, DP);
-    addjob(1, w_h, wh_p, D, D, DP, DP);
-    addjob(2, w_d1, wd1_p, D, D, DP, DP);
-    addjob(3, w_d2, wd2_p, D, D, DP, DP);
-    addjob(4, a_dT, adT_p, D, D, DP, DP);
-    addjob(5, a_dG, adG_p, D, D, DP, DP);
-    addjob(6, a_lT, alT_p, D, D, DP, DP);
-    addjob(7, a_lG, alG_p, D, D, DP, DP);
-    addjob(8, w_d3, wcd_p, D, D, DP, DP);
-    addjob(9, w_d4, wcd_p + (size_t)DP * DP, D, D, DP, DP);
-    addjob(10, w_d4 + (size_t)D * D, wcd_p + (size_t)2 * DP * DP, D, D, DP, DP);
-    addjob(11, w_l1, wcl_p, D, D, DP, DP);
-    addjob(12, w_l2, wcl_p + (size_t)DP * DP, D, D, DP, DP);
-    addjob(13, w_l2 + (size_t)D * D, wcl_p + (size_t)2 * DP * DP, D, D, DP, DP);
-    addjob(14, emb, emb_p, VOCAB, D, VOCAB, DP);
-    addjob(15, u_l, ul_p, D, VOCAB, DP, VP);
-    pa.total = cum;
-
-    k_prep<<<2048, 256, 0, stream>>>(pa);
+    addw(0, wz,   D, D, KP_D, 0, KP_D, WT_N, oWZ);
+    addw(1, w_h,  D, D, KP_D, 0, KP_D, WT_N, oWH);
+    addw(2, w_d1, D, D, KP_D, 0, KP_D, WT_N, oWD1);
+    addw(3, w_d2, D, D, KP_D, 0, KP_D, WT_N, oWD2);
+    addw(4, a_dT, D, D, KP_D, 0, KP_D, WT_N, oADT);
+    addw(5, a_dG, D, D, KP_D, 0, KP_D, WT_N, oADG);
+    addw(6, a_lT, D, D, KP_D, 0, KP_D, WT_N, oALT);
+    addw(7, a_lG, D, D, KP_D, 0, KP_D, WT_N, oALG);
+    addw(8,  w_d3,                 D, D, CATP, 0,   KP_D, WT_N, oWCD);
+    addw(9,  w_d4,                 D, D, CATP, 480, KP_D, WT_N, oWCD);
+    addw(10, w_d4 + (size_t)D * D, D, D, CATP, 960, KP_D, WT_N, oWCD);
+    addw(11, w_l1,                 D, D, CATP, 0,   KP_D, WT_N, oWCL);
+    addw(12, w_l2,                 D, D, CATP, 480, KP_D, WT_N, oWCL);
+    addw(13, w_l2 + (size_t)D * D, D, D, CATP, 960, KP_D, WT_N, oWCL);
+    addw(14, emb, VOCAB, D, KP_V, 0, KP_V, WT_N, oEMB);
+    addw(15, u_l, D, VOCAB, KP_D, 0, KP_D, WT_NV, oUL);
+    wa.total = cum;
+
+    k_prepw<<<4096, 256, 0, stream>>>(wa, whi, wlo);
     k_init<<<(BGR * DP + 255) / 256, 256, 0, stream>>>(sumh, root_slot, counter, dl, out);
     k_scatter_roots<<<(BGR + 255) / 256, 256, 0, stream>>>(root_eids, root_slot);
-    k_build_tasks<<<(NELG + 255) / 256, 256, 0, stream>>>(lg_src, lg_dst, edge_src, root_slot, tasks, counter);
-    kA<<<dim3((BGR + CAP) / 64, 8), 256, 0, stream>>>(id_onehot, emb_p, edge_src, root_eids,
-                                                      tasks, counter, f_all);
-    kB<<<dim3(16 + CAP / 64, 8), 256, 0, stream>>>(f_all, wz_p, wh_p, wd1_p, bz, b_h,
-                                                   tasks, counter, catl, fw1, sumh);
-    kC<<<dim3(16, 8), 256, 0, stream>>>(fw1, sumh, root_slot, root_eids, wd2_p, b_d1, catd);
-    kD<<<dim3(16, 8, 2), 256, 0, stream>>>(catd, catl, adT_p, adG_p, alT_p, alG_p,
+    k_build_tasks<<<(NELG + 255) / 256, 256, 0, stream>>>(lg_src, lg_dst, edge_src,
+                                                          root_slot, tasks, counter);
+    k_gather_idoh<<<4096, 256, 0, stream>>>(id_onehot, edge_src, root_eids, tasks,
+                                            counter, idohH, idohL);
+    kA<<<dim3((BGR + CAP) / 64, 8), 256, 0, stream>>>(idohH, idohL, whi + oEMB, wlo + oEMB,
+                                                      counter, fH, fL);
+    kB<<<dim3((BGR + CAP) / 64, 8), 256, 0, stream>>>(fH, fL, whi + oWZ, wlo + oWZ,
+                                                      whi + oWH, wlo + oWH, bz, b_h,
+                                                      tasks, counter, clH, clL, sumh);
+    kB2<<<dim3(16, 8), 256, 0, stream>>>(fH, fL, whi + oWD1, wlo + oWD1, fw1);
+    k_conv_sumh<<<(BGR * KP_D + 255) / 256, 256, 0, stream>>>(sumh, root_slot, root_eids, sH, sL);
+    kC<<<dim3(16, 8), 256, 0, stream>>>(sH, sL, whi + oWD2, wlo + oWD2, fw1, b_d1, cdH, cdL);
+    kD<<<dim3(16, 8, 2), 256, 0, stream>>>(cdH, cdL, clH, clL,
+                                           whi + oADT, wlo + oADT, whi + oADG, wlo + oADG,
+                                           whi + oALT, wlo + oALT, whi + oALG, wlo + oALG,
                                            qdT, qdG, qlT, qlG);
-    k_att<<<2 * BGR, 256, 0, stream>>>(x_T, x_G, gid_T, gid_G, qdT, qdG, qlT, qlG, catd, catl);
-    kEF<<<dim3(16, 8, 2), 256, 0, stream>>>(catd, catl, wcd_p, wcl_p, b_d2, u_d, b_l1, h_l, dl);
+    k_att<<<2 * BGR, 256, 0, stream>>>(x_T, x_G, gid_T, gid_G, qdT, qdG, qlT, qlG,
+                                       cdH, cdL, clH, clL);
+    kEF<<<dim3(16, 8, 2), 256, 0, stream>>>(cdH, cdL, clH, clL,
+                                            whi + oWCD, wlo + oWCD, whi + oWCL, wlo + oWCL,
+                                            b_d2, u_d, b_l1, hlH, hlL, dl);
     k_topo_final<<<1, 1024, 0, stream>>>(dl, b_d3, topo_t, out);
-    kG<<<dim3(16, VP / 64 + 1, 1), 256, 0, stream>>>(h_l, ul_p, b_l2, logits);
+    kG<<<dim3(16, 13), 256, 0, stream>>>(hlH, hlL, whi + oUL, wlo + oUL, b_l2, logits);
     k_ce<<<BGR / 4, 256, 0, stream>>>(logits, label_t, out);
 }
```

Measured after the change: 834.4 us. 1.13x faster.
